# Optimization experiments

Hardware: AMD Instinct MI355X
Metric: run time of the kernel (lower is better)

Reference implementation:

```python
import jax, jax.numpy as jnp
import numpy as np

N, L2, C = 4096, 49, 128   # lmax=6 -> (lmax+1)**2 = 49
RES = 18                   # grid resolution (beta, alpha)


def setup_inputs() -> dict:
    key = jax.random.key(0)
    k1, k2, k3 = jax.random.split(key, 3)
    inputs = jax.random.normal(k1, (N, L2, C), dtype=jnp.float32)
    # Stand-ins for the precomputed spherical-harmonic transform matrices
    # (to_grid_mat / from_grid_mat), shape (res_beta, res_alpha, (lmax+1)**2).
    W_to = jax.random.normal(k2, (RES, RES, L2), dtype=jnp.float32) / jnp.sqrt(jnp.float32(L2))
    W_from = jax.random.normal(k3, (RES, RES, L2), dtype=jnp.float32) / jnp.sqrt(jnp.float32(RES * RES))
    return {"inputs": inputs, "W_to": W_to, "W_from": W_from}


def reference(inputs, W_to, W_from):
    # to_grid: coefficients -> real-space S2 grid  (n, beta, alpha, c)
    grid = jnp.einsum('bai,nic->nbac', W_to, inputs)
    # elementwise self tensor product on the grid
    grid = grid * grid
    # from_grid: project back to spherical-harmonic coefficients (n, i, c)
    outputs = jnp.einsum('bai,nbac->nic', W_from, grid)
    return outputs
```

## Files before the change

kernel.cpp:

```cpp
#include <hip/hip_runtime.h>
#include <hip/hip_bf16.h>


#define NN    4096
#define L2D   49
#define CCH   128
#define GTOT  324
#define MT1P  22
#define KC2   11

typedef __attribute__((ext_vector_type(8))) short bf16x8;
typedef __attribute__((ext_vector_type(4))) float f32x4;

#define WT_SHORTS (MT1P * 2 * 64 * 8)
#define WF_SHORTS (4 * KC2 * 64 * 8)

__device__ __forceinline__ short f2bf(float f) {
    union { float f; unsigned u; } x; x.f = f;
    return (short)((x.u + 0x7fffu + ((x.u >> 16) & 1u)) >> 16);
}

__device__ __forceinline__ unsigned pack2bf(float a, float b) {
    __hip_bfloat162 p = __float22bfloat162_rn(make_float2(a, b));
    union { __hip_bfloat162 h; unsigned u; } c; c.h = p;
    return c.u;
}

__global__ void prep_w_kernel(const float* __restrict__ Wt,
                              const float* __restrict__ Wf,
                              short* __restrict__ WtF,
                              short* __restrict__ WfF)
{
    int idx = blockIdx.x * 256 + threadIdx.x;
    if (idx < WT_SHORTS) {
        int j = idx & 7, lane = (idx >> 3) & 63, kcx = (idx >> 9) & 1, mt = idx >> 10;
        int g = mt * 16 + (lane & 15);
        int i = kcx * 32 + (lane >> 4) * 8 + j;
        WtF[idx] = f2bf((g < GTOT && i < L2D) ? Wt[g * L2D + i] : 0.0f);
    } else if (idx < WT_SHORTS + WF_SHORTS) {
        int e = idx - WT_SHORTS;
        int j = e & 7, lane = (e >> 3) & 63, t = e >> 9;
        int kc2 = t % KC2, it = t / KC2;
        int i = it * 16 + (lane & 15);
        int g = kc2 * 32 + (j >> 2) * 16 + (lane >> 4) * 4 + (j & 3);
        WfF[e] = f2bf((g < GTOT && i < L2D) ? Wf[g * L2D + i] : 0.0f);
    }
}

__global__ __launch_bounds__(256, 2)
void stp_mfma3_kernel(const float* __restrict__ inp,
                      const short* __restrict__ WtF,
                      const short* __restrict__ WfF,
                      float* __restrict__ out)
{
    const int tid  = threadIdx.x;
    const int lane = tid & 63;
    const int wave = tid >> 6;
    const int lm   = lane & 15;
    const int quad = lane >> 4;

    const int task = blockIdx.x * 4 + wave;
    const int np   = task >> 1;
    const int h    = task & 1;
    const int n0   = np * 2;

    bf16x8 Bx[2][4][2];
    #pragma unroll
    for (int nn = 0; nn < 2; ++nn) {
        const float* __restrict__ Xn = inp + (size_t)(n0 + nn) * (L2D * CCH);
        #pragma unroll
        for (int t = 0; t < 4; ++t) {
            const int c = h * 64 + t * 16 + lm;
            #pragma unroll
            for (int kcx = 0; kcx < 2; ++kcx) {
                union { bf16x8 v; unsigned u[4]; } pk;
                #pragma unroll
                for (int d = 0; d < 4; ++d) {
                    const int i0 = kcx * 32 + quad * 8 + 2 * d;
                    float a = (i0     < L2D) ? Xn[(i0    ) * CCH + c] : 0.0f;
                    float b = (i0 + 1 < L2D) ? Xn[(i0 + 1) * CCH + c] : 0.0f;
                    pk.u[d] = pack2bf(a, b);
                }
                Bx[nn][t][kcx] = pk.v;
            }
        }
    }

    f32x4 acc2[2][4][4];
    #pragma unroll
    for (int nn = 0; nn < 2; ++nn)
        #pragma unroll
        for (int it = 0; it < 4; ++it)
            #pragma unroll
            for (int t = 0; t < 4; ++t)
                acc2[nn][it][t] = (f32x4){0.0f, 0.0f, 0.0f, 0.0f};

    #pragma unroll 1
    for (int kc2 = 0; kc2 < KC2; ++kc2) {
        bf16x8 Wtf[2][2];
        #pragma unroll
        for (int tt = 0; tt < 2; ++tt)
            #pragma unroll
            for (int kcx = 0; kcx < 2; ++kcx)
                Wtf[tt][kcx] = *(const bf16x8*)&WtF[(((2 * kc2 + tt) * 2 + kcx) * 64 + lane) * 8];
        bf16x8 Wff[4];
        #pragma unroll
        for (int it = 0; it < 4; ++it)
            Wff[it] = *(const bf16x8*)&WfF[((it * KC2 + kc2) * 64 + lane) * 8];

        #pragma unroll
        for (int nn = 0; nn < 2; ++nn) {
            #pragma unroll
            for (int t = 0; t < 4; ++t) {
                union { bf16x8 v; unsigned u[4]; } bg;
                #pragma unroll
                for (int tt = 0; tt < 2; ++tt) {
                    f32x4 g = (f32x4){0.0f, 0.0f, 0.0f, 0.0f};
                    g = __builtin_amdgcn_mfma_f32_16x16x32_bf16(Wtf[tt][0], Bx[nn][t][0], g, 0, 0, 0);
                    g = __builtin_amdgcn_mfma_f32_16x16x32_bf16(Wtf[tt][1], Bx[nn][t][1], g, 0, 0, 0);
                    bg.u[tt * 2 + 0] = pack2bf(g[0] * g[0], g[1] * g[1]);
                    bg.u[tt * 2 + 1] = pack2bf(g[2] * g[2], g[3] * g[3]);
                }
                #pragma unroll
                for (int it = 0; it < 4; ++it)
                    acc2[nn][it][t] = __builtin_amdgcn_mfma_f32_16x16x32_bf16(Wff[it], bg.v, acc2[nn][it][t], 0, 0, 0);
            }
        }
    }

    #pragma unroll
    for (int nn = 0; nn < 2; ++nn) {
        float* __restrict__ On = out + (size_t)(n0 + nn) * (L2D * CCH);
        #pragma unroll
        for (int it = 0; it < 4; ++it) {
            #pragma unroll
            for (int t = 0; t < 4; ++t) {
                const int c = h * 64 + t * 16 + lm;
                #pragma unroll
                for (int r = 0; r < 4; ++r) {
                    const int i = it * 16 + quad * 4 + r;
                    if (i < L2D) __builtin_nontemporal_store(acc2[nn][it][t][r], &On[i * CCH + c]);
                }
            }
        }
    }
}

extern "C" void kernel_launch(void* const* d_in, const int* in_sizes, int n_in,
                              void* d_out, int out_size, void* d_ws, size_t ws_size,
                              hipStream_t stream) {
    const float* inp = (const float*)d_in[0];
    const float* Wt  = (const float*)d_in[1];
    const float* Wf  = (const float*)d_in[2];
    float* out = (float*)d_out;

    short* WtF = (short*)d_ws;
    short* WfF = WtF + WT_SHORTS;

    const int prep_threads = WT_SHORTS + WF_SHORTS;
    prep_w_kernel<<<(prep_threads + 255) / 256, 256, 0, stream>>>(Wt, Wf, WtF, WfF);
    stp_mfma3_kernel<<<1024, 256, 0, stream>>>(inp, WtF, WfF, out);
}
```

Measured before the change: 242.1 us.

## Stage weight fragments in LDS with double-buffered async loads, one sample per wave

Weight fragments for each k-chunk are now copied cooperatively into a double-buffered shared-memory array with global_load_lds, with the next chunk prefetched while the current one is consumed. Each wave previously read all fragments from global memory on its own; now a block shares them. Each wave handles one sample instead of two, which halves the accumulator registers, raises the launch-bounds occupancy hint from 2 to 3, and doubles the grid to 2048 blocks. In exchange it adds a block-wide barrier per iteration and does less work per wave, so the weight loads are amortized over fewer MFMAs.

New measurement: 231.6 us. -4.4%, faster.

```diff
diff --git a/kernel.cpp b/kernel.cpp
--- a/kernel.cpp
+++ b/kernel.cpp
@@ -8,6 +8,7 @@
 #define GTOT  324
 #define MT1P  22
 #define KC2   11
+#define FRAG_SHORTS 512
 
 typedef __attribute__((ext_vector_type(8))) short bf16x8;
 typedef __attribute__((ext_vector_type(4))) float f32x4;
@@ -47,100 +48,115 @@
     }
 }
 
-__global__ __launch_bounds__(256, 2)
-void stp_mfma3_kernel(const float* __restrict__ inp,
+__global__ __launch_bounds__(256, 3)
+void stp_mfma4_kernel(const float* __restrict__ inp,
                       const short* __restrict__ WtF,
                       const short* __restrict__ WfF,
                       float* __restrict__ out)
 {
+    __shared__ __align__(16) short Wbuf[2][8 * FRAG_SHORTS];
+
     const int tid  = threadIdx.x;
     const int lane = tid & 63;
     const int wave = tid >> 6;
     const int lm   = lane & 15;
     const int quad = lane >> 4;
 
-    const int task = blockIdx.x * 4 + wave;
-    const int np   = task >> 1;
-    const int h    = task & 1;
-    const int n0   = np * 2;
+    const int h = blockIdx.x & 1;
+    const int n = (blockIdx.x >> 1) * 4 + wave;
 
-    bf16x8 Bx[2][4][2];
+    const float* __restrict__ Xn = inp + (size_t)n * (L2D * CCH);
+
+    #define STAGE(buf, kc)                                                          \
+        {                                                                           \
+            _Pragma("unroll")                                                       \
+            for (int p = 0; p < 2; ++p) {                                           \
+                const int f = wave * 2 + p;                                         \
+                const short* src = (f < 4)                                          \
+                    ? (WtF + ((2 * (kc) + (f >> 1)) * 2 + (f & 1)) * FRAG_SHORTS)   \
+                    : (WfF + ((f - 4) * KC2 + (kc)) * FRAG_SHORTS);                 \
+                __builtin_amdgcn_global_load_lds(                                   \
+                    (const __attribute__((address_space(1))) void*)(src + lane * 8),\
+                    (__attribute__((address_space(3))) void*)(&Wbuf[(buf)][f * FRAG_SHORTS]), \
+                    16, 0, 0);                                                      \
+            }                                                                       \
+        }
+
+    STAGE(0, 0);
+
+    bf16x8 Bx[4][2];
     #pragma unroll
-    for (int nn = 0; nn < 2; ++nn) {
-        const float* __restrict__ Xn = inp + (size_t)(n0 + nn) * (L2D * CCH);
+    for (int t = 0; t < 4; ++t) {
+        const int c = h * 64 + t * 16 + lm;
         #pragma unroll
-        for (int t = 0; t < 4; ++t) {
-            const int c = h * 64 + t * 16 + lm;
+        for (int kcx = 0; kcx < 2; ++kcx) {
+            union { bf16x8 v; unsigned u[4]; } pk;
             #pragma unroll
-            for (int kcx = 0; kcx < 2; ++kcx) {
-                union { bf16x8 v; unsigned u[4]; } pk;
-                #pragma unroll
-                for (int d = 0; d < 4; ++d) {
-                    const int i0 = kcx * 32 + quad * 8 + 2 * d;
-                    float a = (i0     < L2D) ? Xn[(i0    ) * CCH + c] : 0.0f;
-                    float b = (i0 + 1 < L2D) ? Xn[(i0 + 1) * CCH + c] : 0.0f;
-                    pk.u[d] = pack2bf(a, b);
-                }
-                Bx[nn][t][kcx] = pk.v;
+            for (int d = 0; d < 4; ++d) {
+                const int i0 = kcx * 32 + quad * 8 + 2 * d;
+                float a = (i0     < L2D) ? Xn[(i0    ) * CCH + c] : 0.0f;
+                float b = (i0 + 1 < L2D) ? Xn[(i0 + 1) * CCH + c] : 0.0f;
+                pk.u[d] = pack2bf(a, b);
             }
+            Bx[t][kcx] = pk.v;
         }
     }
 
-    f32x4 acc2[2][4][4];
+    f32x4 acc2[4][4];
     #pragma unroll
-    for (int nn = 0; nn < 2; ++nn)
+    for (int it = 0; it < 4; ++it)
         #pragma unroll
-        for (int it = 0; it < 4; ++it)
-            #pragma unroll
-            for (int t = 0; t < 4; ++t)
-                acc2[nn][it][t] = (f32x4){0.0f, 0.0f, 0.0f, 0.0f};
+        for (int t = 0; t < 4; ++t)
+            acc2[it][t] = (f32x4){0.0f, 0.0f, 0.0f, 0.0f};
 
+    __syncthreads();
+
+    int b = 0;
     #pragma unroll 1
     for (int kc2 = 0; kc2 < KC2; ++kc2) {
+        if (kc2 + 1 < KC2) STAGE(b ^ 1, kc2 + 1);
+
+        const short* __restrict__ Wb = &Wbuf[b][0];
         bf16x8 Wtf[2][2];
         #pragma unroll
         for (int tt = 0; tt < 2; ++tt)
             #pragma unroll
             for (int kcx = 0; kcx < 2; ++kcx)
-                Wtf[tt][kcx] = *(const bf16x8*)&WtF[(((2 * kc2 + tt) * 2 + kcx) * 64 + lane) * 8];
+                Wtf[tt][kcx] = *(const bf16x8*)&Wb[(tt * 2 + kcx) * FRAG_SHORTS + lane * 8];
         bf16x8 Wff[4];
         #pragma unroll
         for (int it = 0; it < 4; ++it)
-            Wff[it] = *(const bf16x8*)&WfF[((it * KC2 + kc2) * 64 + lane) * 8];
+            Wff[it] = *(const bf16x8*)&Wb[(4 + it) * FRAG_SHORTS + lane * 8];
 
         #pragma unroll
-        for (int nn = 0; nn < 2; ++nn) {
+        for (int t = 0; t < 4; ++t) {
+            union { bf16x8 v; unsigned u[4]; } bg;
             #pragma unroll
-            for (int t = 0; t < 4; ++t) {
-                union { bf16x8 v; unsigned u[4]; } bg;
-                #pragma unroll
-                for (int tt = 0; tt < 2; ++tt) {
-                    f32x4 g = (f32x4){0.0f, 0.0f, 0.0f, 0.0f};
-                    g = __builtin_amdgcn_mfma_f32_16x16x32_bf16(Wtf[tt][0], Bx[nn][t][0], g, 0, 0, 0);
-                    g = __builtin_amdgcn_mfma_f32_16x16x32_bf16(Wtf[tt][1], Bx[nn][t][1], g, 0, 0, 0);
-                    bg.u[tt * 2 + 0] = pack2bf(g[0] * g[0], g[1] * g[1]);
-                    bg.u[tt * 2 + 1] = pack2bf(g[2] * g[2], g[3] * g[3]);
-                }
-                #pragma unroll
-                for (int it = 0; it < 4; ++it)
-                    acc2[nn][it][t] = __builtin_amdgcn_mfma_f32_16x16x32_bf16(Wff[it], bg.v, acc2[nn][it][t], 0, 0, 0);
+            for (int tt = 0; tt < 2; ++tt) {
+                f32x4 g = (f32x4){0.0f, 0.0f, 0.0f, 0.0f};
+                g = __builtin_amdgcn_mfma_f32_16x16x32_bf16(Wtf[tt][0], Bx[t][0], g, 0, 0, 0);
+                g = __builtin_amdgcn_mfma_f32_16x16x32_bf16(Wtf[tt][1], Bx[t][1], g, 0, 0, 0);
+                bg.u[tt * 2 + 0] = pack2bf(g[0] * g[0], g[1] * g[1]);
+                bg.u[tt * 2 + 1] = pack2bf(g[2] * g[2], g[3] * g[3]);
             }
+            #pragma unroll
+            for (int it = 0; it < 4; ++it)
+                acc2[it][t] = __builtin_amdgcn_mfma_f32_16x16x32_bf16(Wff[it], bg.v, acc2[it][t], 0, 0, 0);
         }
+        __syncthreads();
+        b ^= 1;
     }
 
+    float* __restrict__ On = out + (size_t)n * (L2D * CCH);
     #pragma unroll
-    for (int nn = 0; nn < 2; ++nn) {
-        float* __restrict__ On = out + (size_t)(n0 + nn) * (L2D * CCH);
+    for (int it = 0; it < 4; ++it) {
         #pragma unroll
-        for (int it = 0; it < 4; ++it) {
+        for (int t = 0; t < 4; ++t) {
+            const int c = h * 64 + t * 16 + lm;
             #pragma unroll
-            for (int t = 0; t < 4; ++t) {
-                const int c = h * 64 + t * 16 + lm;
-                #pragma unroll
-                for (int r = 0; r < 4; ++r) {
-                    const int i = it * 16 + quad * 4 + r;
-                    if (i < L2D) __builtin_nontemporal_store(acc2[nn][it][t][r], &On[i * CCH + c]);
-                }
+            for (int r = 0; r < 4; ++r) {
+                const int i = it * 16 + quad * 4 + r;
+                if (i < L2D) __builtin_nontemporal_store(acc2[it][t][r], &On[i * CCH + c]);
             }
         }
     }
@@ -159,5 +175,5 @@
 
     const int prep_threads = WT_SHORTS + WF_SHORTS;
     prep_w_kernel<<<(prep_threads + 255) / 256, 256, 0, stream>>>(Wt, Wf, WtF, WfF);
-    stp_mfma3_kernel<<<1024, 256, 0, stream>>>(inp, WtF, WfF, out);
+    stp_mfma4_kernel<<<2048, 256, 0, stream>>>(inp, WtF, WfF, out);
 }
```
